# Kernel tuning notes

Hardware: AMD Instinct MI355X
Metric: run time of the kernel (lower is better)

Reference implementation:

```python
import jax, jax.numpy as jnp
import numpy as np
from jax import lax

IC, OC, K = 512, 512, 3
EPS = 1e-8
BLUR = np.array([1.0, 3.0, 3.0, 1.0], dtype=np.float32)


def setup_inputs() -> dict:
    key = jax.random.key(0)
    k1, k2 = jax.random.split(key)
    x = jax.random.normal(k1, (1, IC, 128, 128), dtype=jnp.float32)
    weight = jax.random.normal(k2, (1, OC, IC, K, K), dtype=jnp.float32)
    return {"x": x, "weight": weight}


def _blur_kernel():
    k1d = BLUR / BLUR.sum()  # normalize before outer product is equiv (sum of outer = 1)
    k2d = np.outer(k1d, k1d)
    k2d = k2d / k2d.sum()
    k2d = k2d * 4.0  # upsample_factor ** 2
    return jnp.asarray(k2d, dtype=jnp.float32)


def reference(x, weight):
    # x: (1, IC, H, W); weight: (1, OC, IC, K, K)
    scale = 1.0 / np.sqrt(IC * K * K)
    w = scale * weight
    # demodulation (batch = 1)
    demod = lax.rsqrt(jnp.sum(w * w, axis=(2, 3, 4)) + EPS)  # (1, OC)
    w = w * demod[:, :, None, None, None]
    w = w[0]  # (OC, IC, K, K)

    # conv_transpose2d(stride=2, padding=0) == conv with lhs_dilation=2,
    # spatial pad K-1, and spatially-flipped kernel.
    wt = jnp.flip(w, axis=(2, 3))  # (OC, IC, K, K)
    out = lax.conv_general_dilated(
        x, wt,
        window_strides=(1, 1),
        padding=[(K - 1, K - 1), (K - 1, K - 1)],
        lhs_dilation=(2, 2),
        dimension_numbers=("NCHW", "OIHW", "NCHW"),
    )  # (1, OC, 2H+1, 2W+1) = (1, 512, 257, 257)

    # Blur: depthwise FIR filter, pad0 = pad1 = 1, kernel 4x4 (upfirdn2d flips kernel)
    bk = jnp.flip(_blur_kernel(), axis=(0, 1))  # (4, 4), symmetric so flip is a no-op
    bkern = jnp.broadcast_to(bk[None, None], (OC, 1, 4, 4))
    out = lax.conv_general_dilated(
        out, bkern,
        window_strides=(1, 1),
        padding=[(1, 1), (1, 1)],
        feature_group_count=OC,
        dimension_numbers=("NCHW", "OIHW", "NCHW"),
    )  # (1, OC, 256, 256)
    return out
```

## Files before the change

### kernel.cpp

```cpp
#include <hip/hip_runtime.h>
#include <hip/hip_bf16.h>

#define ICN 512
#define OCN 512
#define RS    136
#define NROW  17792
#define GUARD 144
#define XROWS 17936

typedef __attribute__((ext_vector_type(8))) short short8;
typedef __attribute__((ext_vector_type(4))) float f32x4;

__device__ __forceinline__ void gload_lds16(const void* g, void* l) {
  __builtin_amdgcn_global_load_lds(
      (const __attribute__((address_space(1))) void*)g,
      (__attribute__((address_space(3))) void*)l, 16, 0, 0);
}

__device__ __forceinline__ void bar_raw() {
  asm volatile("" ::: "memory");
  __builtin_amdgcn_s_barrier();
  asm volatile("" ::: "memory");
}

__global__ __launch_bounds__(256) void wprep_k(const float* __restrict__ w,
                                               __hip_bfloat16* __restrict__ AP) {
  constexpr int WIDX[9] = {0, 2, 6, 8, 1, 7, 3, 5, 4};
  const int oc = blockIdx.x;
  const int tid = threadIdx.x, lane = tid & 63, wv = tid >> 6;

  float v[2][9];
  float s = 0.f;
#pragma unroll
  for (int rep = 0; rep < 2; ++rep) {
    const int ic = tid + rep * 256;
    const float* wp = w + ((size_t)oc * ICN + ic) * 9;
#pragma unroll
    for (int j = 0; j < 9; ++j) { v[rep][j] = wp[j]; s += wp[j] * wp[j]; }
  }
#pragma unroll
  for (int o = 32; o > 0; o >>= 1) s += __shfl_down(s, o, 64);
  __shared__ float red[4];
  if (lane == 0) red[wv] = s;
  __syncthreads();
  const float tot = red[0] + red[1] + red[2] + red[3];
  const float scale2 = 1.0f / 4608.0f;
  const float c = sqrtf(scale2) * rsqrtf(scale2 * tot + 1e-8f);

#pragma unroll
  for (int rep = 0; rep < 2; ++rep) {
    const int ic = tid + rep * 256;
#pragma unroll
    for (int tp = 0; tp < 9; ++tp)
      AP[((size_t)tp * OCN + oc) * ICN + ic] = __float2bfloat16(c * v[rep][WIDX[tp]]);
  }
}

__global__ __launch_bounds__(256) void packx2_k(const float* __restrict__ x,
                                                unsigned int* __restrict__ XP32) {
  const int py  = blockIdx.x;
  const int ic0 = blockIdx.y * 64;
  const int tid = threadIdx.x;
  const int yy  = py - 1;
  const bool rowvalid = (unsigned)yy < 128u;

  __shared__ __hip_bfloat16 T[128 * 65];

  if (rowvalid) {
    const float4* xr = (const float4*)(x + (size_t)ic0 * 16384 + (size_t)yy * 128);
#pragma unroll
    for (int rep = 0; rep < 8; ++rep) {
      const int idx = rep * 256 + tid;
      const int x4 = idx & 31, ici = idx >> 5;
      const float4 v = xr[(size_t)ici * 4096 + x4];
      const int xx = x4 * 4;
      T[(xx + 0) * 65 + ici] = __float2bfloat16(v.x);
      T[(xx + 1) * 65 + ici] = __float2bfloat16(v.y);
      T[(xx + 2) * 65 + ici] = __float2bfloat16(v.z);
      T[(xx + 3) * 65 + ici] = __float2bfloat16(v.w);
    }
  }
  __syncthreads();

  const size_t rowbase = (size_t)(GUARD + py * 136) * 256 + (ic0 >> 1);
  for (int rep = 0; rep < 17; ++rep) {
    const int idx = rep * 256 + tid;
    const int px = idx >> 5, j = idx & 31;
    unsigned int uv = 0;
    if (rowvalid && (unsigned)(px - 1) < 128u) {
      union { __hip_bfloat16 h[2]; unsigned int u; } cv;
      cv.h[0] = T[(px - 1) * 65 + 2 * j];
      cv.h[1] = T[(px - 1) * 65 + 2 * j + 1];
      uv = cv.u;
    }
    XP32[rowbase + (size_t)px * 256 + j] = uv;
  }
}

__global__ __launch_bounds__(256) void zguard_k(unsigned int* __restrict__ XP32) {
  const int r = blockIdx.x;
  const int row = (r < 144) ? r : (r + 17680);
  XP32[(size_t)row * 256 + threadIdx.x] = 0;
}

__global__ __launch_bounds__(512, 2) void gemm_k(const __hip_bfloat16* __restrict__ AP,
                                                 const __hip_bfloat16* __restrict__ XPT,
                                                 __hip_bfloat16* __restrict__ C) {
  constexpr int NTt[4]   = {4, 2, 2, 1};
  constexpr int TPO[4]   = {0, 4, 6, 8};
  constexpr int SHIFT[9] = {0, 1, 136, 137, 0, 136, 0, 1, 0};
  constexpr int AR[4]    = {129, 129, 128, 128};
  constexpr int AC[4]    = {129, 128, 129, 128};

  const int n0 = blockIdx.x * 256, oc0 = blockIdx.y * 256, ph = blockIdx.z;
  const int tid = threadIdx.x, lane = tid & 63, wv = tid >> 6;
  const int wr = wv >> 2, wc = wv & 3;
  const int lane15 = lane & 15, l7 = lane & 7;
  const int kx = (lane >> 4) * 16;

  __shared__ __align__(16) char lds[2 * 65536];

  const int T = NTt[ph] * 8;

  auto STAGE = [&](int i, char* Lb) {
    const int tp = TPO[ph] + (i >> 3);
    const size_t kb = (size_t)(i & 7) * 128;
    const char* Ag = (const char*)AP + (size_t)tp * (512 * 1024) +
                     (size_t)oc0 * 1024 + kb;
    const char* Bg = (const char*)XPT +
                     (size_t)(GUARD + n0 - SHIFT[tp]) * 1024 + kb;
#pragma unroll
    for (int hh = 0; hh < 2; ++hh)
#pragma unroll
      for (int c = 0; c < 2; ++c) {
        const int d = c * 8192 + tid * 16;
        const int r = d >> 7;
        const int wk = (d & 127) ^ ((r & 7) << 4);
        gload_lds16(Ag + (size_t)(hh * 128 + r) * 1024 + wk,
                    Lb + hh * 16384 + c * 8192 + wv * 1024);
        gload_lds16(Bg + (size_t)(hh * 128 + r) * 1024 + wk,
                    Lb + 32768 + hh * 16384 + c * 8192 + wv * 1024);
      }
  };

  f32x4 acc[8][4];
#pragma unroll
  for (int m = 0; m < 8; ++m)
#pragma unroll
    for (int n = 0; n < 4; ++n) acc[m][n] = (f32x4){0.f, 0.f, 0.f, 0.f};

  STAGE(0, lds);
  asm volatile("s_waitcnt vmcnt(0)" ::: "memory");
  bar_raw();

  for (int t = 0; t < T; ++t) {
    const int buf = t & 1;
    const char* LA = lds + buf * 65536 + wr * 16384;
    const char* LB = lds + buf * 65536 + 32768 + (wc >> 1) * 16384;
    const int brow = (wc & 1) * 64;

    short8 bf[4][2], afA[2][2], afB[2][2];

#pragma unroll
    for (int n = 0; n < 4; ++n)
#pragma unroll
      for (int kh = 0; kh < 2; ++kh) {
        const int e = (brow + n * 16 + lane15) * 128 + kh * 64 + kx;
        bf[n][kh] = *(const short8*)(LB + (e ^ (l7 << 4)));
      }
#pragma unroll
    for (int j = 0; j < 2; ++j)
#pragma unroll
      for (int kh = 0; kh < 2; ++kh) {
        const int e = ((0 + j) * 16 + lane15) * 128 + kh * 64 + kx;
        afA[j][kh] = *(const short8*)(LA + (e ^ (l7 << 4)));
      }
    if (t + 1 < T) STAGE(t + 1, lds + (buf ^ 1) * 65536);
    bar_raw();
    asm volatile("s_waitcnt lgkmcnt(0)");
    __builtin_amdgcn_sched_barrier(0);
    __builtin_amdgcn_s_setprio(1);
#pragma unroll
    for (int j = 0; j < 2; ++j)
#pragma unroll
      for (int kh = 0; kh < 2; ++kh)
#pragma unroll
        for (int n = 0; n < 4; ++n)
          acc[0 + j][n] = __builtin_amdgcn_mfma_f32_16x16x32_bf16(afA[j][kh], bf[n][kh], acc[0 + j][n], 0, 0, 0);
    __builtin_amdgcn_s_setprio(0);
    bar_raw();

#pragma unroll
    for (int j = 0; j < 2; ++j)
#pragma unroll
      for (int kh = 0; kh < 2; ++kh) {
        const int e = ((2 + j) * 16 + lane15) * 128 + kh * 64 + kx;
        afB[j][kh] = *(const short8*)(LA + (e ^ (l7 << 4)));
      }
    bar_raw();
    asm volatile("s_waitcnt lgkmcnt(0)");
    __builtin_amdgcn_sched_barrier(0);
    __builtin_amdgcn_s_setprio(1);
#pragma unroll
    for (int j = 0; j < 2; ++j)
#pragma unroll
      for (int kh = 0; kh < 2; ++kh)
#pragma unroll
        for (int n = 0; n < 4; ++n)
          acc[2 + j][n] = __builtin_amdgcn_mfma_f32_16x16x32_bf16(afB[j][kh], bf[n][kh], acc[2 + j][n], 0, 0, 0);
    __builtin_amdgcn_s_setprio(0);
    bar_raw();

#pragma unroll
    for (int j = 0; j < 2; ++j)
#pragma unroll
      for (int kh = 0; kh < 2; ++kh) {
        const int e = ((4 + j) * 16 + lane15) * 128 + kh * 64 + kx;
        afA[j][kh] = *(const short8*)(LA + (e ^ (l7 << 4)));
      }
    bar_raw();
    asm volatile("s_waitcnt lgkmcnt(0)");
    __builtin_amdgcn_sched_barrier(0);
    __builtin_amdgcn_s_setprio(1);
#pragma unroll
    for (int j = 0; j < 2; ++j)
#pragma unroll
      for (int kh = 0; kh < 2; ++kh)
#pragma unroll
        for (int n = 0; n < 4; ++n)
          acc[4 + j][n] = __builtin_amdgcn_mfma_f32_16x16x32_bf16(afA[j][kh], bf[n][kh], acc[4 + j][n], 0, 0, 0);
    __builtin_amdgcn_s_setprio(0);
    bar_raw();

#pragma unroll
    for (int j = 0; j < 2; ++j)
#pragma unroll
      for (int kh = 0; kh < 2; ++kh) {
        const int e = ((6 + j) * 16 + lane15) * 128 + kh * 64 + kx;
        afB[j][kh] = *(const short8*)(LA + (e ^ (l7 << 4)));
      }
    bar_raw();
    asm volatile("s_waitcnt lgkmcnt(0)");
    __builtin_amdgcn_sched_barrier(0);
    __builtin_amdgcn_s_setprio(1);
#pragma unroll
    for (int j = 0; j < 2; ++j)
#pragma unroll
      for (int kh = 0; kh < 2; ++kh)
#pragma unroll
        for (int n = 0; n < 4; ++n)
          acc[6 + j][n] = __builtin_amdgcn_mfma_f32_16x16x32_bf16(afB[j][kh], bf[n][kh], acc[6 + j][n], 0, 0, 0);
    __builtin_amdgcn_s_setprio(0);
    asm volatile("s_waitcnt vmcnt(0)" ::: "memory");
    __builtin_amdgcn_sched_barrier(0);
    bar_raw();
  }

  const int lr = (lane >> 4) * 4, lc = lane & 15;
#pragma unroll
  for (int n = 0; n < 4; ++n) {
    const int col = n0 + wc * 64 + n * 16 + lc;
    if (col < NROW) {
      const int pa = col / 136, pb = col - pa * 136;
      const bool ok = ((unsigned)(pa - 1) < (unsigned)AR[ph]) &&
                      ((unsigned)(pb - 1) < (unsigned)AC[ph]);
#pragma unroll
      for (int m = 0; m < 8; ++m)
#pragma unroll
        for (int r = 0; r < 4; ++r) {
          const int row = oc0 + wr * 128 + m * 16 + lr + r;
          C[((size_t)(ph * OCN + row)) * NROW + col] =
              __float2bfloat16(ok ? acc[m][n][r] : 0.f);
        }
    }
  }
}

struct __align__(8) U4 { unsigned int w[4]; };

__global__ __launch_bounds__(256) void blur2_k(const unsigned short* __restrict__ C,
                                               float* __restrict__ out) {
  const int tid = threadIdx.x;
  const int t  = tid & 31;
  const int m  = blockIdx.x * 8 + (tid >> 5);
  const int oc = blockIdx.y;
  const float cfv[4] = {0.25f, 0.75f, 0.75f, 0.25f};

  float acc[8];
#pragma unroll
  for (int s = 0; s < 8; ++s) acc[s] = 0.f;

#pragma unroll
  for (int i = 0; i < 4; ++i) {
    const int u  = m - 1 + i;
    const int py = u & 1;
    const int r  = (u >> 1) + 1;
    const size_t base = (size_t)r * 136 + 4 * t;
    const U4 ev = *(const U4*)(C + ((size_t)(py * 2 + 0) * OCN + oc) * NROW + base);
    const U4 ov = *(const U4*)(C + ((size_t)(py * 2 + 1) * OCN + oc) * NROW + base);
    float E[8], O[8];
#pragma unroll
    for (int j = 0; j < 4; ++j) {
      E[2 * j]     = __uint_as_float(ev.w[j] << 16);
      E[2 * j + 1] = __uint_as_float(ev.w[j] & 0xffff0000u);
      O[2 * j]     = __uint_as_float(ov.w[j] << 16);
      O[2 * j + 1] = __uint_as_float(ov.w[j] & 0xffff0000u);
    }
    const float cv = cfv[i];
#pragma unroll
    for (int s = 0; s < 8; ++s) {
      float h;
      if ((s & 1) == 0) {
        const int k = s >> 1;
        h = 0.75f * E[k + 1] + 0.25f * E[k + 2] + 0.25f * O[k] + 0.75f * O[k + 1];
      } else {
        const int k = (s + 1) >> 1;
        h = 0.25f * E[k] + 0.75f * E[k + 1] + 0.75f * O[k] + 0.25f * O[k + 1];
      }
      acc[s] += cv * h;
    }
  }

  float* op = out + ((size_t)oc * 256 + m) * 256 + 8 * t;
  f32x4 s0 = {acc[0], acc[1], acc[2], acc[3]};
  f32x4 s1 = {acc[4], acc[5], acc[6], acc[7]};
  *(f32x4*)op = s0;
  *(f32x4*)(op + 4) = s1;
}

extern "C" void kernel_launch(void* const* d_in, const int* in_sizes, int n_in,
                              void* d_out, int out_size, void* d_ws, size_t ws_size,
                              hipStream_t stream) {
  const float* x = (const float*)d_in[0];
  const float* w = (const float*)d_in[1];
  float* out = (float*)d_out;

  __hip_bfloat16* AP  = (__hip_bfloat16*)d_ws;
  __hip_bfloat16* XPT = (__hip_bfloat16*)((char*)d_ws + 4718592);
  __hip_bfloat16* C   = (__hip_bfloat16*)((char*)d_ws + 23085056);

  wprep_k<<<512, 256, 0, stream>>>(w, AP);
  zguard_k<<<256, 256, 0, stream>>>((unsigned int*)XPT);
  packx2_k<<<dim3(130, 8), 256, 0, stream>>>(x, (unsigned int*)XPT);
  gemm_k<<<dim3(70, 2, 4), 512, 0, stream>>>(AP, XPT, C);
  blur2_k<<<dim3(32, 512), 256, 0, stream>>>((const unsigned short*)C, out);
}
```

Baseline: 155.1 us.

## Remove intra-iteration barriers and double-buffer A fragments with partial lgkmcnt waits

Drops the per-phase s_barrier calls inside the main K loop and double-buffers the A-operand register fragments, so the next fragment's LDS reads are issued before the current MFMA group runs and only a partial lgkmcnt wait is used. The global-to-LDS stage for the next tile is now always issued, and on the last iteration it reloads tile T-1, which avoids a branch at the cost of one redundant load. This is meant to cut barrier stalls and hide LDS latency behind MFMA work, at the cost of more live registers. Correctness depends on the lgkmcnt counts matching the actual number of outstanding LDS operations.

```diff
diff --git a/kernel.cpp b/kernel.cpp
--- a/kernel.cpp
+++ b/kernel.cpp
@@ -159,7 +159,7 @@
     const char* LB = lds + buf * 65536 + 32768 + (wc >> 1) * 16384;
     const int brow = (wc & 1) * 64;
 
-    short8 bf[4][2], afA[2][2], afB[2][2];
+    short8 bf[4][2], af0[2][2], af1[2][2];
 
 #pragma unroll
     for (int n = 0; n < 4; ++n)
@@ -173,10 +173,78 @@
 #pragma unroll
       for (int kh = 0; kh < 2; ++kh) {
         const int e = ((0 + j) * 16 + lane15) * 128 + kh * 64 + kx;
-        afA[j][kh] = *(const short8*)(LA + (e ^ (l7 << 4)));
-      }
-    if (t + 1 < T) STAGE(t + 1, lds + (buf ^ 1) * 65536);
-    bar_raw();
+        af0[j][kh] = *(const short8*)(LA + (e ^ (l7 << 4)));
+      }
+    __builtin_amdgcn_sched_barrier(0);
+    {
+      const int ts = (t + 1 < T) ? (t + 1) : (T - 1);
+      STAGE(ts, lds + (buf ^ 1) * 65536);
+    }
+    __builtin_amdgcn_sched_barrier(0);
+#pragma unroll
+    for (int j = 0; j < 2; ++j)
+#pragma unroll
+      for (int kh = 0; kh < 2; ++kh) {
+        const int e = ((2 + j) * 16 + lane15) * 128 + kh * 64 + kx;
+        af1[j][kh] = *(const short8*)(LA + (e ^ (l7 << 4)));
+      }
+    __builtin_amdgcn_sched_barrier(0);
+
+    asm volatile("s_waitcnt lgkmcnt(4)");
+    __builtin_amdgcn_sched_barrier(0);
+    __builtin_amdgcn_s_setprio(1);
+#pragma unroll
+    for (int j = 0; j < 2; ++j)
+#pragma unroll
+      for (int kh = 0; kh < 2; ++kh)
+#pragma unroll
+        for (int n = 0; n < 4; ++n)
+          acc[0 + j][n] = __builtin_amdgcn_mfma_f32_16x16x32_bf16(af0[j][kh], bf[n][kh], acc[0 + j][n], 0, 0, 0);
+    __builtin_amdgcn_s_setprio(0);
+    __builtin_amdgcn_sched_barrier(0);
+
+#pragma unroll
+    for (int j = 0; j < 2; ++j)
+#pragma unroll
+      for (int kh = 0; kh < 2; ++kh) {
+        const int e = ((4 + j) * 16 + lane15) * 128 + kh * 64 + kx;
+        af0[j][kh] = *(const short8*)(LA + (e ^ (l7 << 4)));
+      }
+    __builtin_amdgcn_sched_barrier(0);
+    asm volatile("s_waitcnt lgkmcnt(4)");
+    __builtin_amdgcn_sched_barrier(0);
+    __builtin_amdgcn_s_setprio(1);
+#pragma unroll
+    for (int j = 0; j < 2; ++j)
+#pragma unroll
+      for (int kh = 0; kh < 2; ++kh)
+#pragma unroll
+        for (int n = 0; n < 4; ++n)
+          acc[2 + j][n] = __builtin_amdgcn_mfma_f32_16x16x32_bf16(af1[j][kh], bf[n][kh], acc[2 + j][n], 0, 0, 0);
+    __builtin_amdgcn_s_setprio(0);
+    __builtin_amdgcn_sched_barrier(0);
+
+#pragma unroll
+    for (int j = 0; j < 2; ++j)
+#pragma unroll
+      for (int kh = 0; kh < 2; ++kh) {
+        const int e = ((6 + j) * 16 + lane15) * 128 + kh * 64 + kx;
+        af1[j][kh] = *(const short8*)(LA + (e ^ (l7 << 4)));
+      }
+    __builtin_amdgcn_sched_barrier(0);
+    asm volatile("s_waitcnt lgkmcnt(4)");
+    __builtin_amdgcn_sched_barrier(0);
+    __builtin_amdgcn_s_setprio(1);
+#pragma unroll
+    for (int j = 0; j < 2; ++j)
+#pragma unroll
+      for (int kh = 0; kh < 2; ++kh)
+#pragma unroll
+        for (int n = 0; n < 4; ++n)
+          acc[4 + j][n] = __builtin_amdgcn_mfma_f32_16x16x32_bf16(af0[j][kh], bf[n][kh], acc[4 + j][n], 0, 0, 0);
+    __builtin_amdgcn_s_setprio(0);
+    __builtin_amdgcn_sched_barrier(0);
+
     asm volatile("s_waitcnt lgkmcnt(0)");
     __builtin_amdgcn_sched_barrier(0);
     __builtin_amdgcn_s_setprio(1);
@@ -186,71 +254,9 @@
       for (int kh = 0; kh < 2; ++kh)
 #pragma unroll
         for (int n = 0; n < 4; ++n)
-          acc[0 + j][n] = __builtin_amdgcn_mfma_f32_16x16x32_bf16(afA[j][kh], bf[n][kh], acc[0 + j][n], 0, 0, 0);
+          acc[6 + j][n] = __builtin_amdgcn_mfma_f32_16x16x32_bf16(af1[j][kh], bf[n][kh], acc[6 + j][n], 0, 0, 0);
     __builtin_amdgcn_s_setprio(0);
-    bar_raw();
-
-#pragma unroll
-    for (int j = 0; j < 2; ++j)
-#pragma unroll
-      for (int kh = 0; kh < 2; ++kh) {
-        const int e = ((2 + j) * 16 + lane15) * 128 + kh * 64 + kx;
-        afB[j][kh] = *(const short8*)(LA + (e ^ (l7 << 4)));
-      }
-    bar_raw();
-    asm volatile("s_waitcnt lgkmcnt(0)");
-    __builtin_amdgcn_sched_barrier(0);
-    __builtin_amdgcn_s_setprio(1);
-#pragma unroll
-    for (int j = 0; j < 2; ++j)
-#pragma unroll
-      for (int kh = 0; kh < 2; ++kh)
-#pragma unroll
-        for (int n = 0; n < 4; ++n)
-          acc[2 + j][n] = __builtin_amdgcn_mfma_f32_16x16x32_bf16(afB[j][kh], bf[n][kh], acc[2 + j][n], 0, 0, 0);
-    __builtin_amdgcn_s_setprio(0);
-    bar_raw();
-
-#pragma unroll
-    for (int j = 0; j < 2; ++j)
-#pragma unroll
-      for (int kh = 0; kh < 2; ++kh) {
-        const int e = ((4 + j) * 16 + lane15) * 128 + kh * 64 + kx;
-        afA[j][kh] = *(const short8*)(LA + (e ^ (l7 << 4)));
-      }
-    bar_raw();
-    asm volatile("s_waitcnt lgkmcnt(0)");
-    __builtin_amdgcn_sched_barrier(0);
-    __builtin_amdgcn_s_setprio(1);
-#pragma unroll
-    for (int j = 0; j < 2; ++j)
-#pragma unroll
-      for (int kh = 0; kh < 2; ++kh)
-#pragma unroll
-        for (int n = 0; n < 4; ++n)
-          acc[4 + j][n] = __builtin_amdgcn_mfma_f32_16x16x32_bf16(afA[j][kh], bf[n][kh], acc[4 + j][n], 0, 0, 0);
-    __builtin_amdgcn_s_setprio(0);
-    bar_raw();
-
-#pragma unroll
-    for (int j = 0; j < 2; ++j)
-#pragma unroll
-      for (int kh = 0; kh < 2; ++kh) {
-        const int e = ((6 + j) * 16 + lane15) * 128 + kh * 64 + kx;
-        afB[j][kh] = *(const short8*)(LA + (e ^ (l7 << 4)));
-      }
-    bar_raw();
-    asm volatile("s_waitcnt lgkmcnt(0)");
-    __builtin_amdgcn_sched_barrier(0);
-    __builtin_amdgcn_s_setprio(1);
-#pragma unroll
-    for (int j = 0; j < 2; ++j)
-#pragma unroll
-      for (int kh = 0; kh < 2; ++kh)
-#pragma unroll
-        for (int n = 0; n < 4; ++n)
-          acc[6 + j][n] = __builtin_amdgcn_mfma_f32_16x16x32_bf16(afB[j][kh], bf[n][kh], acc[6 + j][n], 0, 0, 0);
-    __builtin_amdgcn_s_setprio(0);
+
     asm volatile("s_waitcnt vmcnt(0)" ::: "memory");
     __builtin_amdgcn_sched_barrier(0);
     bar_raw();
```

Result: faster. 146.0 us (-5.9%).
